# Kernel optimization log

Hardware: AMD Instinct MI355X
Metric: run time of the kernel (lower is better)

Reference implementation:

```python
import jax, jax.numpy as jnp
import numpy as np

N = 50000        # nodes
E = 1_600_000    # edges
F_IN = 128
HID = 128
OUT = 128
NEG_SLOPE = 0.2  # PyG GATConv default


def _gat_layer(x, src, dst, W, a_src, a_dst, b, n_nodes):
    """PyG GATConv (heads=1, add_self_loops handled by caller)."""
    h = x @ W                                   # [N, d_out]
    alpha_src = h @ a_src                       # [N]
    alpha_dst = h @ a_dst                       # [N]
    e = jax.nn.leaky_relu(alpha_src[src] + alpha_dst[dst], NEG_SLOPE)  # [E']
    # segment softmax over incoming edges of each destination node
    m = jax.ops.segment_max(e, dst, num_segments=n_nodes)
    e = jnp.exp(e - m[dst])
    s = jax.ops.segment_sum(e, dst, num_segments=n_nodes)
    alpha = e / s[dst]                          # [E']
    out = jax.ops.segment_sum(alpha[:, None] * h[src], dst, num_segments=n_nodes)
    return out + b


def setup_inputs() -> dict:
    key = jax.random.key(0)
    ks = jax.random.split(key, 11)
    sW1 = 1.0 / np.sqrt(F_IN)
    sW2 = 1.0 / np.sqrt(HID)
    return {
        "x": jax.random.normal(ks[0], (N, F_IN), dtype=jnp.float32),
        "edge_index": jax.random.randint(ks[1], (2, E), 0, N, dtype=jnp.int64
                                         if jax.config.jax_enable_x64 else jnp.int32),
        "W1": jax.random.normal(ks[2], (F_IN, HID), dtype=jnp.float32) * sW1,
        "a1_src": jax.random.normal(ks[3], (HID,), dtype=jnp.float32) * sW2,
        "a1_dst": jax.random.normal(ks[4], (HID,), dtype=jnp.float32) * sW2,
        "b1": jnp.zeros((HID,), dtype=jnp.float32),
        "W2": jax.random.normal(ks[5], (HID, OUT), dtype=jnp.float32) * sW2,
        "a2_src": jax.random.normal(ks[6], (OUT,), dtype=jnp.float32) * sW2,
        "a2_dst": jax.random.normal(ks[7], (OUT,), dtype=jnp.float32) * sW2,
        "b2": jnp.zeros((OUT,), dtype=jnp.float32),
    }


def reference(x, edge_index, W1, a1_src, a1_dst, b1, W2, a2_src, a2_dst, b2):
    n = x.shape[0]
    loop = jnp.arange(n, dtype=edge_index.dtype)
    src = jnp.concatenate([edge_index[0], loop])   # add self loops (PyG default)
    dst = jnp.concatenate([edge_index[1], loop])
    h = _gat_layer(x, src, dst, W1, a1_src, a1_dst, b1, n)
    h = jax.nn.relu(h)
    # F.dropout with training=False is identity (eval-mode reference)
    out = _gat_layer(h, src, dst, W2, a2_src, a2_dst, b2, n)
    return out
```

## Files before the change

### kernel.cpp

```cpp
#include <hip/hip_runtime.h>
#include <hip/hip_bf16.h>
#include <hip/hip_fp16.h>

#define FD 128
#define CBW 128
#define NBK 512

typedef _Float16 half8 __attribute__((ext_vector_type(8)));
typedef float f32x4 __attribute__((ext_vector_type(4)));

__global__ __launch_bounds__(256) void k_wz(const float* __restrict__ W1,
                                            const float* __restrict__ W2,
                                            __half* __restrict__ T1,
                                            __half* __restrict__ T2,
                                            int* __restrict__ ccnt, int nb) {
    const int t = threadIdx.x;
    if (blockIdx.x == 2) {
        for (int i = t; i < nb; i += 256) ccnt[i] = 0;
        return;
    }
    __shared__ float sw[128 * 129];
    const float* W = blockIdx.x ? W2 : W1;
    __half* T = blockIdx.x ? T2 : T1;
#pragma unroll
    for (int i = 0; i < 64; i++) {
        int idx = i * 256 + t;
        sw[(idx >> 7) * 129 + (idx & 127)] = W[idx];
    }
    __syncthreads();
#pragma unroll
    for (int i = 0; i < 32; i++) {
        int o = i * 256 + t;
        int c = o >> 6, kp = o & 63;
        float lo = sw[(kp * 2) * 129 + c];
        float hi = sw[(kp * 2 + 1) * 129 + c];
        *(__half2*)&T[c * 128 + kp * 2] = __floats2half2_rn(lo, hi);
    }
}

__device__ __forceinline__ void gemm_core(const half8 A[4],
                                          const __half* __restrict__ Wt,
                                          const float* __restrict__ a_s,
                                          const float* __restrict__ a_d,
                                          __half* __restrict__ H,
                                          float* __restrict__ as_,
                                          float* __restrict__ ad_,
                                          int n, int row0, int g, int c16) {
    f32x4 acc[8];
#pragma unroll
    for (int ct = 0; ct < 8; ct++) acc[ct] = (f32x4){0.f, 0.f, 0.f, 0.f};
#pragma unroll
    for (int ct = 0; ct < 8; ct++) {
        const __half* wp = &Wt[(ct * 16 + c16) * 128 + g * 8];
#pragma unroll
        for (int kc = 0; kc < 4; kc++) {
            half8 b = *(const half8*)(wp + kc * 32);
            acc[ct] = __builtin_amdgcn_mfma_f32_16x16x32_f16(A[kc], b, acc[ct], 0, 0, 0);
        }
    }
    float asv[8], adv[8];
#pragma unroll
    for (int ct = 0; ct < 8; ct++) {
        asv[ct] = a_s[ct * 16 + c16];
        adv[ct] = a_d[ct * 16 + c16];
    }
#pragma unroll
    for (int r = 0; r < 4; r++) {
        const int row = row0 + g * 4 + r;
        float vs = 0.f, vd = 0.f;
#pragma unroll
        for (int ct = 0; ct < 8; ct++) {
            float v = acc[ct][r];
            vs += v * asv[ct];
            vd += v * adv[ct];
            if (row < n) {
                size_t hoff = (size_t)(ct >> 2) * ((size_t)n * 64)
                            + (size_t)row * 64 + (ct & 3) * 16 + c16;
                H[hoff] = __float2half(v);
            }
        }
#pragma unroll
        for (int off = 8; off; off >>= 1) {
            vs += __shfl_xor(vs, off, 16);
            vd += __shfl_xor(vd, off, 16);
        }
        if (c16 == 0 && row < n) { as_[row] = vs; ad_[row] = vd; }
    }
}

__global__ __launch_bounds__(256) void k_pg(const int* __restrict__ dst,
                                            int* __restrict__ ccnt, int e, int nb,
                                            const float* __restrict__ X,
                                            const __half* __restrict__ Wt,
                                            const float* __restrict__ a_s,
                                            const float* __restrict__ a_d,
                                            __half* __restrict__ H,
                                            float* __restrict__ as_,
                                            float* __restrict__ ad_, int n) {
    __shared__ int lh[NBK];
    const int t = threadIdx.x;
    if (blockIdx.x < 256) {
        for (int i = t; i < NBK; i += 256) lh[i] = 0;
        __syncthreads();
        for (int i = blockIdx.x * 256 + t; i < e; i += 256 * 256)
            atomicAdd(&lh[dst[i] >> 7], 1);
        __syncthreads();
        for (int i = t; i < nb; i += 256) {
            int c = lh[i];
            if (c) atomicAdd(&ccnt[i], c);
        }
    } else {
        const int bid = blockIdx.x - 256;
        const int wave = t >> 6, lane = t & 63;
        const int g = lane >> 4, c16 = lane & 15;
        const int row0 = bid * 64 + wave * 16;
        half8 A[4];
        {
            int row = row0 + c16;
            int rc = (row < n) ? row : (n - 1);
            const float* xp = &X[(size_t)rc * 128 + g * 8];
#pragma unroll
            for (int kc = 0; kc < 4; kc++) {
                float4 x0 = *(const float4*)(xp + kc * 32);
                float4 x1 = *(const float4*)(xp + kc * 32 + 4);
                half8 a;
                a[0] = (_Float16)x0.x; a[1] = (_Float16)x0.y;
                a[2] = (_Float16)x0.z; a[3] = (_Float16)x0.w;
                a[4] = (_Float16)x1.x; a[5] = (_Float16)x1.y;
                a[6] = (_Float16)x1.z; a[7] = (_Float16)x1.w;
                A[kc] = a;
            }
        }
        gemm_core(A, Wt, a_s, a_d, H, as_, ad_, n, row0, g, c16);
    }
}

__global__ void k_cscan(const int* __restrict__ ccnt, int* __restrict__ cbase,
                        int* __restrict__ ccur, int nb, int* __restrict__ rowptr, int n) {
    __shared__ int wsum[16];
    __shared__ int woff[17];
    const int t = threadIdx.x, lane = t & 63, wid = t >> 6;
    int v = (t < nb) ? ccnt[t] : 0;
    int s = v;
#pragma unroll
    for (int off = 1; off < 64; off <<= 1) {
        int u = __shfl_up(s, off, 64);
        if (lane >= off) s += u;
    }
    if (lane == 63) wsum[wid] = s;
    __syncthreads();
    if (wid == 0) {
        int w2 = (lane < 16) ? wsum[lane] : 0;
#pragma unroll
        for (int off = 1; off < 16; off <<= 1) {
            int u = __shfl_up(w2, off, 64);
            if (lane >= off) w2 += u;
        }
        if (lane < 16) woff[lane + 1] = w2;
        if (lane == 0) woff[0] = 0;
    }
    __syncthreads();
    int excl = woff[wid] + (s - v);
    if (t < nb) { cbase[t] = excl; ccur[t] = excl; }
    if (t == 0) { cbase[nb] = woff[16]; rowptr[n] = woff[16]; }
}

__global__ __launch_bounds__(256) void k_scat(const int* __restrict__ src,
                                              const int* __restrict__ dst,
                                              int* __restrict__ ccur,
                                              int* __restrict__ ebuf,
                                              int e, int nb, int nscat) {
    __shared__ int lh[NBK];
    __shared__ int lb[NBK];
    const int t = threadIdx.x;
    const int per = (e + nscat - 1) / nscat;
    const int lo = blockIdx.x * per;
    const int hi = min(e, lo + per);
    for (int i = t; i < NBK; i += 256) lh[i] = 0;
    __syncthreads();
    for (int i = lo + t; i < hi; i += 256) atomicAdd(&lh[dst[i] >> 7], 1);
    __syncthreads();
    for (int i = t; i < nb; i += 256) {
        int c = lh[i];
        lb[i] = c ? atomicAdd(&ccur[i], c) : 0;
    }
    __syncthreads();
    for (int i = t; i < NBK; i += 256) lh[i] = 0;
    __syncthreads();
    for (int i = lo + t; i < hi; i += 256) {
        int d = dst[i];
        int bkt = d >> 7;
        int r = atomicAdd(&lh[bkt], 1);
        ebuf[lb[bkt] + r] = (src[i] << 7) | (d & (CBW - 1));
    }
}

__global__ __launch_bounds__(256) void k_fine(const int* __restrict__ ebuf,
                                              const int* __restrict__ cbase,
                                              int* __restrict__ rowptr,
                                              int* __restrict__ colidx, int n) {
    const int b = blockIdx.x;
    const int node0 = b * CBW;
    const int nloc = min(CBW, n - node0);
    const int beg = cbase[b], end = cbase[b + 1];
    __shared__ int fh[CBW];
    __shared__ int fo[CBW];
    __shared__ int w0tot;
    const int t = threadIdx.x;
    if (t < CBW) fh[t] = 0;
    __syncthreads();
    for (int e = beg + t; e < end; e += 256) atomicAdd(&fh[ebuf[e] & (CBW - 1)], 1);
    __syncthreads();
    int v = 0, s = 0;
    if (t < CBW) {
        v = fh[t];
        s = v;
#pragma unroll
        for (int off = 1; off < 64; off <<= 1) {
            int u = __shfl_up(s, off, 64);
            if ((t & 63) >= off) s += u;
        }
        if (t == 63) w0tot = s;
    }
    __syncthreads();
    if (t < CBW) fo[t] = ((t >= 64) ? w0tot : 0) + s - v;
    __syncthreads();
    if (t < nloc) rowptr[node0 + t] = beg + fo[t];
    if (t < CBW) fh[t] = 0;
    __syncthreads();
    for (int e = beg + t; e < end; e += 256) {
        int rec = ebuf[e];
        int d = rec & (CBW - 1);
        int r = atomicAdd(&fh[d], 1);
        colidx[beg + fo[d] + r] = rec >> 7;
    }
}

__global__ __launch_bounds__(256) void k_gemm(const __half* __restrict__ X,
                                              const __half* __restrict__ Wt,
                                              const float* __restrict__ a_s,
                                              const float* __restrict__ a_d,
                                              __half* __restrict__ H,
                                              float* __restrict__ as_,
                                              float* __restrict__ ad_, int n) {
    const int t = threadIdx.x;
    const int wave = t >> 6, lane = t & 63;
    const int g = lane >> 4, c16 = lane & 15;
    const int row0 = blockIdx.x * 64 + wave * 16;
    half8 A[4];
    {
        int row = row0 + c16;
        int rc = (row < n) ? row : (n - 1);
        const __half* xp = &X[(size_t)rc * 128 + g * 8];
#pragma unroll
        for (int kc = 0; kc < 4; kc++) A[kc] = *(const half8*)(xp + kc * 32);
    }
    gemm_core(A, Wt, a_s, a_d, H, as_, ad_, n, row0, g, c16);
}

__device__ __forceinline__ void fmix8(float* acc, uint4 hv, float w) {
    union { uint4 u; _Float16 h[8]; } c;
    c.u = hv;
#pragma unroll
    for (int j = 0; j < 8; j++) acc[j] += w * (float)c.h[j];
}

__global__ __launch_bounds__(256) void k_aggr(const __half* __restrict__ H,
                                              const float* __restrict__ as_,
                                              const float* __restrict__ ad_,
                                              const int* __restrict__ rowptr,
                                              const int* __restrict__ colidx,
                                              const float* __restrict__ bias,
                                              float* __restrict__ outf,
                                              __half* __restrict__ outh,
                                              int n, int mode) {
    __shared__ int2 pr[4][64];
    const int half = blockIdx.x & 1;
    const int nblk = blockIdx.x >> 1;
    const int wid = threadIdx.x >> 6;
    const int lane = threadIdx.x & 63;
    const int node = nblk * 4 + wid;
    if (node >= n) return;
    const int g8 = lane >> 3;
    const int l8 = lane & 7;
    const int boff = l8 * 16;
    const char* Hb = (const char*)H + (size_t)half * ((size_t)n * 128) + boff;
    const float adn = ad_[node];
    float sp = 0.f;
    float acc[8] = {0.f, 0.f, 0.f, 0.f, 0.f, 0.f, 0.f, 0.f};
    const int beg = rowptr[node], end = rowptr[node + 1];

    {
        float e = as_[node] + adn;
        e = (e > 0.f) ? e : 0.2f * e;
        const float w = __expf(e);
        if (lane == 63) sp += w;
        if (g8 == 7) {
            const uint4 hv = *(const uint4*)(Hb + (unsigned)node * 128u);
            fmix8(acc, hv, w);
        }
    }

    for (int it = beg; it < end; it += 64) {
        const int idx = it + lane;
        const bool valid = idx < end;
        const int sl = colidx[valid ? idx : (end - 1)];
        float e = as_[sl] + adn;
        e = (e > 0.f) ? e : 0.2f * e;
        const float w = valid ? __expf(e) : 0.f;
        sp += w;
        pr[wid][lane] = make_int2((int)((unsigned)sl * 128u), __float_as_int(w));
        int m = end - it; if (m > 64) m = 64;
        const int iters = (m + 7) >> 3;
        int slot = g8;
#pragma unroll 4
        for (int g = 0; g < iters; ++g) {
            const int2 p = pr[wid][slot];
            const float wg = __int_as_float(p.y);
            const uint4 hv = *(const uint4*)(Hb + (unsigned)p.x);
            fmix8(acc, hv, wg);
            slot += 8;
        }
    }

#pragma unroll
    for (int off = 1; off < 64; off <<= 1) sp += __shfl_xor(sp, off);
#pragma unroll
    for (int off = 8; off <= 32; off <<= 1) {
#pragma unroll
        for (int j = 0; j < 8; j++) acc[j] += __shfl_xor(acc[j], off);
    }
    if (g8 == 0) {
        const int f0 = half * 64 + l8 * 8;
        const float inv = 1.f / sp;
        float o[8];
        const float4 b0 = *(const float4*)&bias[f0];
        const float4 b1 = *(const float4*)&bias[f0 + 4];
        o[0] = acc[0] * inv + b0.x; o[1] = acc[1] * inv + b0.y;
        o[2] = acc[2] * inv + b0.z; o[3] = acc[3] * inv + b0.w;
        o[4] = acc[4] * inv + b1.x; o[5] = acc[5] * inv + b1.y;
        o[6] = acc[6] * inv + b1.z; o[7] = acc[7] * inv + b1.w;
        if (mode == 1) {
#pragma unroll
            for (int j = 0; j < 8; j++) o[j] = fmaxf(o[j], 0.f);
            union { __half2 h2[4]; uint4 u; } pkk;
            pkk.h2[0] = __floats2half2_rn(o[0], o[1]);
            pkk.h2[1] = __floats2half2_rn(o[2], o[3]);
            pkk.h2[2] = __floats2half2_rn(o[4], o[5]);
            pkk.h2[3] = __floats2half2_rn(o[6], o[7]);
            *(uint4*)&outh[(size_t)node * 128 + f0] = pkk.u;
        } else {
            *(float4*)&outf[(size_t)node * 128 + f0] = make_float4(o[0], o[1], o[2], o[3]);
            *(float4*)&outf[(size_t)node * 128 + f0 + 4] = make_float4(o[4], o[5], o[6], o[7]);
        }
    }
}

extern "C" void kernel_launch(void* const* d_in, const int* in_sizes, int n_in,
                              void* d_out, int out_size, void* d_ws, size_t ws_size,
                              hipStream_t stream) {
    const float* x   = (const float*)d_in[0];
    const int*   ei  = (const int*)d_in[1];
    const float* W1  = (const float*)d_in[2];
    const float* a1s = (const float*)d_in[3];
    const float* a1d = (const float*)d_in[4];
    const float* b1  = (const float*)d_in[5];
    const float* W2  = (const float*)d_in[6];
    const float* a2s = (const float*)d_in[7];
    const float* a2d = (const float*)d_in[8];
    const float* b2  = (const float*)d_in[9];
    float* dout = (float*)d_out;

    const int n = in_sizes[0] / FD;
    const int E = in_sizes[1] / 2;
    const int* src = ei;
    const int* dst = ei + E;
    const int NB = (n + CBW - 1) / CBW;

    char* base = (char*)d_ws;
    __half* buf0  = (__half*)base;
    int*    ebuf  = (int*)base;
    __half* H     = (__half*)(base + (size_t)n * FD * sizeof(__half));
    float* as_    = (float*)((char*)H + (size_t)n * FD * sizeof(__half));
    float* ad_    = as_ + n;
    int*   rowptr = (int*)(ad_ + n);
    int*   ccnt   = rowptr + (n + 1);
    int*   cbase  = ccnt + NB;
    int*   ccur   = cbase + NB + 1;
    int*   colidx = ccur + NB;
    size_t wt_off = (((size_t)((char*)(colidx + E) - base)) + 15) & ~(size_t)15;
    __half* Wt1h  = (__half*)(base + wt_off);
    __half* Wt2h  = Wt1h + 128 * 128;

    const int gemm_grid = (n + 63) / 64;
    const int node_grid = (n + 3) / 4;
    const int SCAT = 256;

    k_wz<<<3, 256, 0, stream>>>(W1, W2, Wt1h, Wt2h, ccnt, NB);
    k_pg<<<256 + gemm_grid, 256, 0, stream>>>(dst, ccnt, E, NB,
                                              x, Wt1h, a1s, a1d, H, as_, ad_, n);
    k_cscan<<<1, 1024, 0, stream>>>(ccnt, cbase, ccur, NB, rowptr, n);
    k_scat<<<SCAT, 256, 0, stream>>>(src, dst, ccur, ebuf, E, NB, SCAT);
    k_fine<<<NB, 256, 0, stream>>>(ebuf, cbase, rowptr, colidx, n);
    k_aggr<<<node_grid * 2, 256, 0, stream>>>(H, as_, ad_, rowptr, colidx, b1,
                                              nullptr, buf0, n, 1);
    k_gemm<<<gemm_grid, 256, 0, stream>>>(buf0, Wt2h, a2s, a2d, H, as_, ad_, n);
    k_aggr<<<node_grid * 2, 256, 0, stream>>>(H, as_, ad_, rowptr, colidx, b2,
                                              dout, nullptr, n, 0);
}
```

Baseline: 223.8 us.

## Precompute per-edge attention weights and softmax normalizers before aggregation

Attention weights are now computed once per edge, in k_fine for layer 1 and in a new k_alpha kernel for layer 2. Each weight is stored as fp16 packed with the 16-bit source index into one 32-bit word, and the per-node inverse sum and self-loop weight are stored alongside. k_aggr then streams these packed words with a simple prefetch loop instead of recomputing exp, reducing sums and staging through shared memory twice per edge (once per feature half). The cost is an extra kernel launch and extra memory traffic for the weight array. Packing the index into 16 bits overflows for node ids of 65536 and above; n is 50000, so it fits here, but it is a latent limitation. Weights are also rounded to fp16.

Result: slower. 239.9 us (+7.2%).

```diff
diff --git a/kernel.cpp b/kernel.cpp
--- a/kernel.cpp
+++ b/kernel.cpp
@@ -198,16 +198,27 @@
 __global__ __launch_bounds__(256) void k_fine(const int* __restrict__ ebuf,
                                               const int* __restrict__ cbase,
                                               int* __restrict__ rowptr,
-                                              int* __restrict__ colidx, int n) {
+                                              int* __restrict__ colidx,
+                                              unsigned* __restrict__ ew,
+                                              const float* __restrict__ as_,
+                                              const float* __restrict__ ad_,
+                                              float* __restrict__ invs,
+                                              float* __restrict__ aself, int n) {
     const int b = blockIdx.x;
     const int node0 = b * CBW;
     const int nloc = min(CBW, n - node0);
     const int beg = cbase[b], end = cbase[b + 1];
     __shared__ int fh[CBW];
     __shared__ int fo[CBW];
+    __shared__ float sums[CBW];
+    __shared__ float lad[CBW];
     __shared__ int w0tot;
     const int t = threadIdx.x;
-    if (t < CBW) fh[t] = 0;
+    if (t < CBW) {
+        fh[t] = 0;
+        sums[t] = 0.f;
+        lad[t] = (t < nloc) ? ad_[node0 + t] : 0.f;
+    }
     __syncthreads();
     for (int e = beg + t; e < end; e += 256) atomicAdd(&fh[ebuf[e] & (CBW - 1)], 1);
     __syncthreads();
@@ -231,8 +242,60 @@
     for (int e = beg + t; e < end; e += 256) {
         int rec = ebuf[e];
         int d = rec & (CBW - 1);
+        int sn = rec >> 7;
         int r = atomicAdd(&fh[d], 1);
-        colidx[beg + fo[d] + r] = rec >> 7;
+        int pos = beg + fo[d] + r;
+        colidx[pos] = sn;
+        float x = as_[sn] + lad[d];
+        x = (x > 0.f) ? x : 0.2f * x;
+        float w = __expf(x);
+        __half hw = __float2half(w);
+        float wq = __half2float(hw);
+        ew[pos] = ((unsigned)sn << 16) | (unsigned)__half_as_ushort(hw);
+        atomicAdd(&sums[d], wq);
+    }
+    __syncthreads();
+    if (t < nloc) {
+        int node = node0 + t;
+        float x = as_[node] + lad[t];
+        x = (x > 0.f) ? x : 0.2f * x;
+        float ws = __expf(x);
+        aself[node] = ws;
+        invs[node] = 1.f / (sums[t] + ws);
+    }
+}
+
+__global__ __launch_bounds__(256) void k_alpha(const float* __restrict__ as_,
+                                               const float* __restrict__ ad_,
+                                               const int* __restrict__ rowptr,
+                                               const int* __restrict__ colidx,
+                                               unsigned* __restrict__ ew,
+                                               float* __restrict__ invs,
+                                               float* __restrict__ aself, int n) {
+    const int wid = threadIdx.x >> 6;
+    const int lane = threadIdx.x & 63;
+    const int node = blockIdx.x * 4 + wid;
+    if (node >= n) return;
+    const float adn = ad_[node];
+    const int beg = rowptr[node], end = rowptr[node + 1];
+    float sp = 0.f;
+    for (int i = beg + lane; i < end; i += 64) {
+        int sn = colidx[i];
+        float x = as_[sn] + adn;
+        x = (x > 0.f) ? x : 0.2f * x;
+        float w = __expf(x);
+        __half hw = __float2half(w);
+        ew[i] = ((unsigned)sn << 16) | (unsigned)__half_as_ushort(hw);
+        sp += __half2float(hw);
+    }
+#pragma unroll
+    for (int off = 32; off; off >>= 1) sp += __shfl_xor(sp, off);
+    if (lane == 0) {
+        float x = as_[node] + adn;
+        x = (x > 0.f) ? x : 0.2f * x;
+        float ws = __expf(x);
+        aself[node] = ws;
+        invs[node] = 1.f / (sp + ws);
     }
 }
 
@@ -266,15 +329,14 @@
 }
 
 __global__ __launch_bounds__(256) void k_aggr(const __half* __restrict__ H,
-                                              const float* __restrict__ as_,
-                                              const float* __restrict__ ad_,
+                                              const unsigned* __restrict__ ew,
+                                              const float* __restrict__ aself,
+                                              const float* __restrict__ invs,
                                               const int* __restrict__ rowptr,
-                                              const int* __restrict__ colidx,
                                               const float* __restrict__ bias,
                                               float* __restrict__ outf,
                                               __half* __restrict__ outh,
                                               int n, int mode) {
-    __shared__ int2 pr[4][64];
     const int half = blockIdx.x & 1;
     const int nblk = blockIdx.x >> 1;
     const int wid = threadIdx.x >> 6;
@@ -283,56 +345,35 @@
     if (node >= n) return;
     const int g8 = lane >> 3;
     const int l8 = lane & 7;
-    const int boff = l8 * 16;
-    const char* Hb = (const char*)H + (size_t)half * ((size_t)n * 128) + boff;
-    const float adn = ad_[node];
-    float sp = 0.f;
+    const char* Hb = (const char*)H + (size_t)half * ((size_t)n * 128) + l8 * 16;
     float acc[8] = {0.f, 0.f, 0.f, 0.f, 0.f, 0.f, 0.f, 0.f};
     const int beg = rowptr[node], end = rowptr[node + 1];
 
-    {
-        float e = as_[node] + adn;
-        e = (e > 0.f) ? e : 0.2f * e;
-        const float w = __expf(e);
-        if (lane == 63) sp += w;
-        if (g8 == 7) {
-            const uint4 hv = *(const uint4*)(Hb + (unsigned)node * 128u);
-            fmix8(acc, hv, w);
-        }
-    }
-
-    for (int it = beg; it < end; it += 64) {
-        const int idx = it + lane;
-        const bool valid = idx < end;
-        const int sl = colidx[valid ? idx : (end - 1)];
-        float e = as_[sl] + adn;
-        e = (e > 0.f) ? e : 0.2f * e;
-        const float w = valid ? __expf(e) : 0.f;
-        sp += w;
-        pr[wid][lane] = make_int2((int)((unsigned)sl * 128u), __float_as_int(w));
-        int m = end - it; if (m > 64) m = 64;
-        const int iters = (m + 7) >> 3;
-        int slot = g8;
-#pragma unroll 4
-        for (int g = 0; g < iters; ++g) {
-            const int2 p = pr[wid][slot];
-            const float wg = __int_as_float(p.y);
-            const uint4 hv = *(const uint4*)(Hb + (unsigned)p.x);
-            fmix8(acc, hv, wg);
-            slot += 8;
-        }
-    }
-
-#pragma unroll
-    for (int off = 1; off < 64; off <<= 1) sp += __shfl_xor(sp, off);
+    if (g8 == 7) {
+        const uint4 hv = *(const uint4*)(Hb + (unsigned)node * 128u);
+        fmix8(acc, hv, aself[node]);
+    }
+
+    int i = beg + g8;
+    unsigned p = (i < end) ? ew[i] : 0u;
+    while (i < end) {
+        const unsigned pc = p;
+        const int i2 = i + 8;
+        if (i2 < end) p = ew[i2];
+        const float w = __half2float(__ushort_as_half((unsigned short)(pc & 0xffffu)));
+        const uint4 hv = *(const uint4*)(Hb + (pc >> 16) * 128u);
+        fmix8(acc, hv, w);
+        i = i2;
+    }
+
 #pragma unroll
     for (int off = 8; off <= 32; off <<= 1) {
 #pragma unroll
         for (int j = 0; j < 8; j++) acc[j] += __shfl_xor(acc[j], off);
     }
     if (g8 == 0) {
+        const float inv = invs[node];
         const int f0 = half * 64 + l8 * 8;
-        const float inv = 1.f / sp;
         float o[8];
         const float4 b0 = *(const float4*)&bias[f0];
         const float4 b1 = *(const float4*)&bias[f0 + 4];
@@ -383,12 +424,15 @@
     __half* H     = (__half*)(base + (size_t)n * FD * sizeof(__half));
     float* as_    = (float*)((char*)H + (size_t)n * FD * sizeof(__half));
     float* ad_    = as_ + n;
-    int*   rowptr = (int*)(ad_ + n);
+    float* invs   = ad_ + n;
+    float* aself  = invs + n;
+    int*   rowptr = (int*)(aself + n);
     int*   ccnt   = rowptr + (n + 1);
     int*   cbase  = ccnt + NB;
     int*   ccur   = cbase + NB + 1;
     int*   colidx = ccur + NB;
-    size_t wt_off = (((size_t)((char*)(colidx + E) - base)) + 15) & ~(size_t)15;
+    unsigned* ew  = (unsigned*)(colidx + E);
+    size_t wt_off = (((size_t)((char*)(ew + E) - base)) + 15) & ~(size_t)15;
     __half* Wt1h  = (__half*)(base + wt_off);
     __half* Wt2h  = Wt1h + 128 * 128;
 
@@ -401,10 +445,12 @@
                                               x, Wt1h, a1s, a1d, H, as_, ad_, n);
     k_cscan<<<1, 1024, 0, stream>>>(ccnt, cbase, ccur, NB, rowptr, n);
     k_scat<<<SCAT, 256, 0, stream>>>(src, dst, ccur, ebuf, E, NB, SCAT);
-    k_fine<<<NB, 256, 0, stream>>>(ebuf, cbase, rowptr, colidx, n);
-    k_aggr<<<node_grid * 2, 256, 0, stream>>>(H, as_, ad_, rowptr, colidx, b1,
+    k_fine<<<NB, 256, 0, stream>>>(ebuf, cbase, rowptr, colidx, ew, as_, ad_,
+                                   invs, aself, n);
+    k_aggr<<<node_grid * 2, 256, 0, stream>>>(H, ew, aself, invs, rowptr, b1,
                                               nullptr, buf0, n, 1);
     k_gemm<<<gemm_grid, 256, 0, stream>>>(buf0, Wt2h, a2s, a2d, H, as_, ad_, n);
-    k_aggr<<<node_grid * 2, 256, 0, stream>>>(H, as_, ad_, rowptr, colidx, b2,
+    k_alpha<<<node_grid, 256, 0, stream>>>(as_, ad_, rowptr, colidx, ew, invs, aself, n);
+    k_aggr<<<node_grid * 2, 256, 0, stream>>>(H, ew, aself, invs, rowptr, b2,
                                               dout, nullptr, n, 0);
 }
```

## Aggregate full 128-wide rows per wave with row-major H and prefetched neighbors

Applied to the files above, without the earlier changes.

The fp16 feature matrix H is now stored row-major with all 128 features contiguous, instead of as two 64-column halves. The aggregation kernel drops its two-blocks-per-node split: each wave now gathers full 256-byte rows, four neighbors at a time, so colidx loads, attention logits and exp are computed once per edge instead of twice. It also prefetches the next 64-edge batch of colidx and source scores during the current batch, and manually unrolls the gather by 4. The trade-off is fewer rows in flight per lane group and a longer per-wave serial loop, with half as many blocks launched.

Result: faster. 210.8 us (-5.8%).

```diff
diff --git a/kernel.cpp b/kernel.cpp
--- a/kernel.cpp
+++ b/kernel.cpp
@@ -73,11 +73,7 @@
             float v = acc[ct][r];
             vs += v * asv[ct];
             vd += v * adv[ct];
-            if (row < n) {
-                size_t hoff = (size_t)(ct >> 2) * ((size_t)n * 64)
-                            + (size_t)row * 64 + (ct & 3) * 16 + c16;
-                H[hoff] = __float2half(v);
-            }
+            if (row < n) H[(size_t)row * 128 + ct * 16 + c16] = __float2half(v);
         }
 #pragma unroll
         for (int off = 8; off; off >>= 1) {
@@ -275,63 +271,90 @@
                                               __half* __restrict__ outh,
                                               int n, int mode) {
     __shared__ int2 pr[4][64];
-    const int half = blockIdx.x & 1;
-    const int nblk = blockIdx.x >> 1;
     const int wid = threadIdx.x >> 6;
     const int lane = threadIdx.x & 63;
-    const int node = nblk * 4 + wid;
+    const int node = blockIdx.x * 4 + wid;
     if (node >= n) return;
-    const int g8 = lane >> 3;
-    const int l8 = lane & 7;
-    const int boff = l8 * 16;
-    const char* Hb = (const char*)H + (size_t)half * ((size_t)n * 128) + boff;
+    const int q = lane >> 4;
+    const int boff = (lane & 15) * 16;
+    const char* Hb = (const char*)H + boff;
     const float adn = ad_[node];
     float sp = 0.f;
     float acc[8] = {0.f, 0.f, 0.f, 0.f, 0.f, 0.f, 0.f, 0.f};
     const int beg = rowptr[node], end = rowptr[node + 1];
+
+    int sl = node;
+    float av = 0.f;
+    if (beg < end) {
+        int idx = beg + lane;
+        sl = colidx[(idx < end) ? idx : (end - 1)];
+        av = as_[sl];
+    }
 
     {
         float e = as_[node] + adn;
         e = (e > 0.f) ? e : 0.2f * e;
         const float w = __expf(e);
         if (lane == 63) sp += w;
-        if (g8 == 7) {
-            const uint4 hv = *(const uint4*)(Hb + (unsigned)node * 128u);
+        if (q == 3) {
+            const uint4 hv = *(const uint4*)(Hb + ((unsigned)node << 8));
             fmix8(acc, hv, w);
         }
     }
 
     for (int it = beg; it < end; it += 64) {
-        const int idx = it + lane;
-        const bool valid = idx < end;
-        const int sl = colidx[valid ? idx : (end - 1)];
-        float e = as_[sl] + adn;
-        e = (e > 0.f) ? e : 0.2f * e;
-        const float w = valid ? __expf(e) : 0.f;
-        sp += w;
-        pr[wid][lane] = make_int2((int)((unsigned)sl * 128u), __float_as_int(w));
+        const int nit = it + 64;
+        int nsl = node; float nav = 0.f;
+        if (nit < end) {
+            int idx2 = nit + lane;
+            nsl = colidx[(idx2 < end) ? idx2 : (end - 1)];
+            nav = as_[nsl];
+        }
+        {
+            const bool valid = (it + lane) < end;
+            float e = av + adn;
+            e = (e > 0.f) ? e : 0.2f * e;
+            const float w = valid ? __expf(e) : 0.f;
+            sp += w;
+            pr[wid][lane] = make_int2((int)((unsigned)sl << 8), __float_as_int(w));
+        }
         int m = end - it; if (m > 64) m = 64;
-        const int iters = (m + 7) >> 3;
-        int slot = g8;
-#pragma unroll 4
-        for (int g = 0; g < iters; ++g) {
+        const int iters = (m + 3) >> 2;
+        int slot = q;
+        int g = 0;
+        for (; g + 4 <= iters; g += 4) {
+            const int2 p0 = pr[wid][slot];
+            const int2 p1 = pr[wid][slot + 4];
+            const int2 p2 = pr[wid][slot + 8];
+            const int2 p3 = pr[wid][slot + 12];
+            const uint4 h0 = *(const uint4*)(Hb + (unsigned)p0.x);
+            const uint4 h1 = *(const uint4*)(Hb + (unsigned)p1.x);
+            const uint4 h2 = *(const uint4*)(Hb + (unsigned)p2.x);
+            const uint4 h3 = *(const uint4*)(Hb + (unsigned)p3.x);
+            fmix8(acc, h0, __int_as_float(p0.y));
+            fmix8(acc, h1, __int_as_float(p1.y));
+            fmix8(acc, h2, __int_as_float(p2.y));
+            fmix8(acc, h3, __int_as_float(p3.y));
+            slot += 16;
+        }
+        for (; g < iters; ++g) {
             const int2 p = pr[wid][slot];
-            const float wg = __int_as_float(p.y);
             const uint4 hv = *(const uint4*)(Hb + (unsigned)p.x);
-            fmix8(acc, hv, wg);
-            slot += 8;
-        }
+            fmix8(acc, hv, __int_as_float(p.y));
+            slot += 4;
+        }
+        sl = nsl; av = nav;
     }
 
 #pragma unroll
     for (int off = 1; off < 64; off <<= 1) sp += __shfl_xor(sp, off);
 #pragma unroll
-    for (int off = 8; off <= 32; off <<= 1) {
+    for (int off = 16; off <= 32; off <<= 1) {
 #pragma unroll
         for (int j = 0; j < 8; j++) acc[j] += __shfl_xor(acc[j], off);
     }
-    if (g8 == 0) {
-        const int f0 = half * 64 + l8 * 8;
+    if (q == 0) {
+        const int f0 = boff >> 1;
         const float inv = 1.f / sp;
         float o[8];
         const float4 b0 = *(const float4*)&bias[f0];
@@ -402,9 +425,9 @@
     k_cscan<<<1, 1024, 0, stream>>>(ccnt, cbase, ccur, NB, rowptr, n);
     k_scat<<<SCAT, 256, 0, stream>>>(src, dst, ccur, ebuf, E, NB, SCAT);
     k_fine<<<NB, 256, 0, stream>>>(ebuf, cbase, rowptr, colidx, n);
-    k_aggr<<<node_grid * 2, 256, 0, stream>>>(H, as_, ad_, rowptr, colidx, b1,
-                                              nullptr, buf0, n, 1);
+    k_aggr<<<node_grid, 256, 0, stream>>>(H, as_, ad_, rowptr, colidx, b1,
+                                          nullptr, buf0, n, 1);
     k_gemm<<<gemm_grid, 256, 0, stream>>>(buf0, Wt2h, a2s, a2d, H, as_, ad_, n);
-    k_aggr<<<node_grid * 2, 256, 0, stream>>>(H, as_, ad_, rowptr, colidx, b2,
-                                              dout, nullptr, n, 0);
-}
+    k_aggr<<<node_grid, 256, 0, stream>>>(H, as_, ad_, rowptr, colidx, b2,
+                                          dout, nullptr, n, 0);
+}
```

## Store H row-major and aggregate full feature rows per wave

Applied to the files above, without the earlier changes.

H moves from two separate 64-feature halves to one row-major 128-feature array. The aggregation kernel now covers all 128 features of a node in a single wave: 16 lanes per row and 4 edges in flight, instead of two blocks per node each handling half the features. This removes the duplicated work of reading colidx and as_ and computing the exp edge weight twice per edge, and each gathered row becomes one contiguous 256-byte read. In exchange each wave has fewer edges in flight and the grid is half as large; the scatter grid is also doubled.

Measured after the change: 205.4 us. -8.2%, faster.

```diff
diff --git a/kernel.cpp b/kernel.cpp
--- a/kernel.cpp
+++ b/kernel.cpp
@@ -73,11 +73,7 @@
             float v = acc[ct][r];
             vs += v * asv[ct];
             vd += v * adv[ct];
-            if (row < n) {
-                size_t hoff = (size_t)(ct >> 2) * ((size_t)n * 64)
-                            + (size_t)row * 64 + (ct & 3) * 16 + c16;
-                H[hoff] = __float2half(v);
-            }
+            if (row < n) H[(size_t)row * 128 + ct * 16 + c16] = __float2half(v);
         }
 #pragma unroll
         for (int off = 8; off; off >>= 1) {
@@ -275,16 +271,13 @@
                                               __half* __restrict__ outh,
                                               int n, int mode) {
     __shared__ int2 pr[4][64];
-    const int half = blockIdx.x & 1;
-    const int nblk = blockIdx.x >> 1;
     const int wid = threadIdx.x >> 6;
     const int lane = threadIdx.x & 63;
-    const int node = nblk * 4 + wid;
+    const int node = blockIdx.x * 4 + wid;
     if (node >= n) return;
-    const int g8 = lane >> 3;
-    const int l8 = lane & 7;
-    const int boff = l8 * 16;
-    const char* Hb = (const char*)H + (size_t)half * ((size_t)n * 128) + boff;
+    const int q = lane >> 4;
+    const int boff = (lane & 15) * 16;
+    const char* Hb = (const char*)H + boff;
     const float adn = ad_[node];
     float sp = 0.f;
     float acc[8] = {0.f, 0.f, 0.f, 0.f, 0.f, 0.f, 0.f, 0.f};
@@ -295,8 +288,8 @@
         e = (e > 0.f) ? e : 0.2f * e;
         const float w = __expf(e);
         if (lane == 63) sp += w;
-        if (g8 == 7) {
-            const uint4 hv = *(const uint4*)(Hb + (unsigned)node * 128u);
+        if (q == 3) {
+            const uint4 hv = *(const uint4*)(Hb + ((unsigned)node << 8));
             fmix8(acc, hv, w);
         }
     }
@@ -309,29 +302,29 @@
         e = (e > 0.f) ? e : 0.2f * e;
         const float w = valid ? __expf(e) : 0.f;
         sp += w;
-        pr[wid][lane] = make_int2((int)((unsigned)sl * 128u), __float_as_int(w));
+        pr[wid][lane] = make_int2((int)((unsigned)sl << 8), __float_as_int(w));
         int m = end - it; if (m > 64) m = 64;
-        const int iters = (m + 7) >> 3;
-        int slot = g8;
+        const int iters = (m + 3) >> 2;
+        int slot = q;
 #pragma unroll 4
         for (int g = 0; g < iters; ++g) {
             const int2 p = pr[wid][slot];
             const float wg = __int_as_float(p.y);
             const uint4 hv = *(const uint4*)(Hb + (unsigned)p.x);
             fmix8(acc, hv, wg);
-            slot += 8;
+            slot += 4;
         }
     }
 
 #pragma unroll
     for (int off = 1; off < 64; off <<= 1) sp += __shfl_xor(sp, off);
 #pragma unroll
-    for (int off = 8; off <= 32; off <<= 1) {
+    for (int off = 16; off <= 32; off <<= 1) {
 #pragma unroll
         for (int j = 0; j < 8; j++) acc[j] += __shfl_xor(acc[j], off);
     }
-    if (g8 == 0) {
-        const int f0 = half * 64 + l8 * 8;
+    if (q == 0) {
+        const int f0 = boff >> 1;
         const float inv = 1.f / sp;
         float o[8];
         const float4 b0 = *(const float4*)&bias[f0];
@@ -394,7 +387,7 @@
 
     const int gemm_grid = (n + 63) / 64;
     const int node_grid = (n + 3) / 4;
-    const int SCAT = 256;
+    const int SCAT = 512;
 
     k_wz<<<3, 256, 0, stream>>>(W1, W2, Wt1h, Wt2h, ccnt, NB);
     k_pg<<<256 + gemm_grid, 256, 0, stream>>>(dst, ccnt, E, NB,
@@ -402,9 +395,9 @@
     k_cscan<<<1, 1024, 0, stream>>>(ccnt, cbase, ccur, NB, rowptr, n);
     k_scat<<<SCAT, 256, 0, stream>>>(src, dst, ccur, ebuf, E, NB, SCAT);
     k_fine<<<NB, 256, 0, stream>>>(ebuf, cbase, rowptr, colidx, n);
-    k_aggr<<<node_grid * 2, 256, 0, stream>>>(H, as_, ad_, rowptr, colidx, b1,
-                                              nullptr, buf0, n, 1);
+    k_aggr<<<node_grid, 256, 0, stream>>>(H, as_, ad_, rowptr, colidx, b1,
+                                          nullptr, buf0, n, 1);
     k_gemm<<<gemm_grid, 256, 0, stream>>>(buf0, Wt2h, a2s, a2d, H, as_, ad_, n);
-    k_aggr<<<node_grid * 2, 256, 0, stream>>>(H, as_, ad_, rowptr, colidx, b2,
-                                              dout, nullptr, n, 0);
-}
+    k_aggr<<<node_grid, 256, 0, stream>>>(H, as_, ad_, rowptr, colidx, b2,
+                                          dout, nullptr, n, 0);
+}
```
